# Performance work log

Hardware: AMD Instinct MI355X
Metric: run time of the kernel (lower is better)

Reference implementation:

```python
import jax, jax.numpy as jnp
import numpy as np
from jax import lax

REPR, ACT, HID = 256, 2, 512
BN_EPS = 1e-5


def setup_inputs() -> dict:
    key = jax.random.key(0)
    ks = jax.random.split(key, 12)
    B, H, W, Tm1 = 512, 64, 64, 16
    d_in = REPR + ACT
    s = lambda k, shape, scale: jax.random.normal(k, shape, dtype=jnp.float32) * scale
    return {
        "init_state": jax.random.normal(ks[0], (B, 2, H, W), dtype=jnp.float32),
        "actions": jax.random.normal(ks[1], (B, Tm1, ACT), dtype=jnp.float32),
        "conv_w": s(ks[2], (16, 2, 3, 3), (1.0 / np.sqrt(2 * 9))),
        "bn_gamma": jnp.ones((16,), jnp.float32),
        "bn_beta": jnp.zeros((16,), jnp.float32),
        "enc_fc_w": s(ks[3], (REPR, 16), (1.0 / np.sqrt(16))),
        "enc_fc_b": s(ks[4], (REPR,), 0.01),
        "gru_w_ih": s(ks[5], (3 * HID, d_in), (1.0 / np.sqrt(HID))),
        "gru_w_hh": s(ks[6], (3 * HID, HID), (1.0 / np.sqrt(HID))),
        "gru_b_ih": s(ks[7], (3 * HID,), (1.0 / np.sqrt(HID))),
        "gru_b_hh": s(ks[8], (3 * HID,), (1.0 / np.sqrt(HID))),
        "pred_fc_w": s(ks[9], (REPR, HID), (1.0 / np.sqrt(HID))),
        "pred_fc_b": s(ks[10], (REPR,), 0.01),
    }


def _encoder(x, conv_w, bn_gamma, bn_beta, enc_fc_w, enc_fc_b):
    # Conv2d(2->16, 3x3, stride 1, pad 1, no bias), NCHW
    y = lax.conv_general_dilated(x, conv_w, (1, 1), "SAME",
                                 dimension_numbers=("NCHW", "OIHW", "NCHW"))
    # BatchNorm2d in training mode: batch statistics over (N, H, W)
    mean = jnp.mean(y, axis=(0, 2, 3), keepdims=True)
    var = jnp.var(y, axis=(0, 2, 3), keepdims=True)
    y = (y - mean) * lax.rsqrt(var + BN_EPS)
    y = y * bn_gamma[None, :, None, None] + bn_beta[None, :, None, None]
    y = jax.nn.relu(y)
    # MaxPool2d(2, 2)
    y = lax.reduce_window(y, -jnp.inf, lax.max, (1, 1, 2, 2), (1, 1, 2, 2), "VALID")
    # AdaptiveAvgPool2d((1,1)) + flatten
    y = jnp.mean(y, axis=(2, 3))  # (B, 16)
    return y @ enc_fc_w.T + enc_fc_b  # (B, repr_dim)


def reference(init_state, actions, conv_w, bn_gamma, bn_beta, enc_fc_w, enc_fc_b,
              gru_w_ih, gru_w_hh, gru_b_ih, gru_b_hh, pred_fc_w, pred_fc_b):
    B = init_state.shape[0]
    s0 = _encoder(init_state, conv_w, bn_gamma, bn_beta, enc_fc_w, enc_fc_b)  # (B, R)

    def step(carry, u_t):
        s_prev, h = carry
        x = jnp.concatenate([s_prev, u_t], axis=-1)          # (B, R+A)
        gx = x @ gru_w_ih.T + gru_b_ih                        # (B, 3H)
        gh = h @ gru_w_hh.T + gru_b_hh                        # (B, 3H)
        gx_r, gx_z, gx_n = jnp.split(gx, 3, axis=-1)
        gh_r, gh_z, gh_n = jnp.split(gh, 3, axis=-1)
        r = jax.nn.sigmoid(gx_r + gh_r)
        z = jax.nn.sigmoid(gx_z + gh_z)
        n = jnp.tanh(gx_n + r * gh_n)
        h_new = (1.0 - z) * n + z * h
        s_pred = jax.nn.relu(h_new @ pred_fc_w.T + pred_fc_b)  # (B, R)
        return (s_pred, h_new), s_pred

    h0 = jnp.zeros((B, HID), dtype=s0.dtype)
    u_seq = jnp.transpose(actions, (1, 0, 2))  # (T-1, B, A)
    _, preds = lax.scan(step, (s0, h0), u_seq)  # preds: (T-1, B, R)
    pred_encs = jnp.concatenate([s0[None], preds], axis=0)  # (T, B, R)
    return jnp.transpose(pred_encs, (1, 0, 2))  # (B, T, R)
```

## Files before the change

### kernel.cpp

```cpp
#include <hip/hip_runtime.h>
#include <hip/hip_bf16.h>
#include <math.h>

#define TM1 16
#define TT 17

typedef __attribute__((ext_vector_type(8))) __bf16 bf16x8;
typedef __attribute__((ext_vector_type(4))) float f32x4;

#define OFF_BSTATS 0
#define OFF_SPB    16384
#define OFF_PWB    81920
#define OFF_WIHB   147456
#define OFF_WHHB   344064
#define OFF_HB     737280

__global__ __launch_bounds__(256) void enc_stats_prep(
    const float* __restrict__ x, const float* __restrict__ cw,
    float* __restrict__ bstats,
    const float* __restrict__ wih, const float* __restrict__ whh,
    const float* __restrict__ pw,
    __hip_bfloat16* __restrict__ wihb, __hip_bfloat16* __restrict__ whhb,
    __hip_bfloat16* __restrict__ pwb) {
  {
    const int n1 = 1536 * 256, n2 = 1536 * 512, n3 = 256 * 512;
    int i = blockIdx.x * 256 + threadIdx.x;
    int st = gridDim.x * 256;
    for (int j = i; j < n1 + n2 + n3; j += st) {
      if (j < n1) {
        int r = j >> 8, c = j & 255;
        wihb[j] = __float2bfloat16(wih[r * 258 + c]);
      } else if (j < n1 + n2) {
        int k = j - n1;
        whhb[k] = __float2bfloat16(whh[k]);
      } else {
        int k = j - n1 - n2;
        pwb[k] = __float2bfloat16(pw[k]);
      }
    }
  }

  __shared__ float imgp[2 * 66 * 66];
  __shared__ float reds[4][16], redq[4][16];
  const int b = blockIdx.x, tid = threadIdx.x;
  const int wv = tid >> 6;
  for (int i = tid; i < 2 * 66 * 66; i += 256) imgp[i] = 0.0f;
  __syncthreads();
  const float* xb = x + b * 8192;
  for (int i = tid; i < 8192; i += 256) {
    int ci = i >> 12, rem = i & 4095, y = rem >> 6, xx = rem & 63;
    imgp[ci * 4356 + (y + 1) * 66 + (xx + 1)] = xb[i];
  }
  __syncthreads();

  for (int c4 = 0; c4 < 4; ++c4) {
    float w0[18], w1[18], w2[18], w3[18];
#pragma unroll
    for (int k = 0; k < 18; ++k) {
      w0[k] = cw[(c4 * 4 + 0) * 18 + k];
      w1[k] = cw[(c4 * 4 + 1) * 18 + k];
      w2[k] = cw[(c4 * 4 + 2) * 18 + k];
      w3[k] = cw[(c4 * 4 + 3) * 18 + k];
    }
    float s0 = 0, s1 = 0, s2 = 0, s3 = 0, q0 = 0, q1 = 0, q2 = 0, q3 = 0;
    for (int p = tid; p < 4096; p += 256) {
      int y = p >> 6, xx = p & 63;
      float v[18];
#pragma unroll
      for (int ci = 0; ci < 2; ++ci)
#pragma unroll
        for (int dy = 0; dy < 3; ++dy)
#pragma unroll
          for (int dx = 0; dx < 3; ++dx)
            v[ci * 9 + dy * 3 + dx] = imgp[ci * 4356 + (y + dy) * 66 + (xx + dx)];
      float a0 = 0, a1 = 0, a2 = 0, a3 = 0;
#pragma unroll
      for (int k = 0; k < 18; ++k) {
        a0 = fmaf(w0[k], v[k], a0);
        a1 = fmaf(w1[k], v[k], a1);
        a2 = fmaf(w2[k], v[k], a2);
        a3 = fmaf(w3[k], v[k], a3);
      }
      s0 += a0; q0 = fmaf(a0, a0, q0);
      s1 += a1; q1 = fmaf(a1, a1, q1);
      s2 += a2; q2 = fmaf(a2, a2, q2);
      s3 += a3; q3 = fmaf(a3, a3, q3);
    }
#pragma unroll
    for (int off = 32; off >= 1; off >>= 1) {
      s0 += __shfl_down(s0, off); q0 += __shfl_down(q0, off);
      s1 += __shfl_down(s1, off); q1 += __shfl_down(q1, off);
      s2 += __shfl_down(s2, off); q2 += __shfl_down(q2, off);
      s3 += __shfl_down(s3, off); q3 += __shfl_down(q3, off);
    }
    if ((tid & 63) == 0) {
      reds[wv][c4 * 4 + 0] = s0; redq[wv][c4 * 4 + 0] = q0;
      reds[wv][c4 * 4 + 1] = s1; redq[wv][c4 * 4 + 1] = q1;
      reds[wv][c4 * 4 + 2] = s2; redq[wv][c4 * 4 + 2] = q2;
      reds[wv][c4 * 4 + 3] = s3; redq[wv][c4 * 4 + 3] = q3;
    }
  }
  __syncthreads();
  if (tid < 16)
    bstats[b * 32 + tid] = reds[0][tid] + reds[1][tid] + reds[2][tid] + reds[3][tid];
  else if (tid < 32) {
    int c = tid - 16;
    bstats[b * 32 + tid] = redq[0][c] + redq[1][c] + redq[2][c] + redq[3][c];
  }
}

__global__ __launch_bounds__(256) void enc_finish(const float* __restrict__ x,
                                                  const float* __restrict__ cw,
                                                  const float* __restrict__ bstats,
                                                  const float* __restrict__ gamma,
                                                  const float* __restrict__ beta,
                                                  const float* __restrict__ fcw,
                                                  const float* __restrict__ fcb,
                                                  __hip_bfloat16* __restrict__ spb,
                                                  float* __restrict__ out) {
  __shared__ float imgp[2 * 66 * 66];
  __shared__ float red[4][16];
  __shared__ float plds[16];
  __shared__ float statsL[32];
  __shared__ float racc[8][32];
  const int b = blockIdx.x, tid = threadIdx.x;

  {
    const int c = tid & 31, part = tid >> 5;
    float s = 0;
    for (int bb = part; bb < 512; bb += 8) s += bstats[bb * 32 + c];
    racc[part][c] = s;
  }
  for (int i = tid; i < 2 * 66 * 66; i += 256) imgp[i] = 0.0f;
  __syncthreads();
  if (tid < 32) {
    float v = 0;
#pragma unroll
    for (int p = 0; p < 8; ++p) v += racc[p][tid];
    statsL[tid] = v;
  }
  const float* xb = x + b * 8192;
  for (int i = tid; i < 8192; i += 256) {
    int ci = i >> 12, rem = i & 4095, y = rem >> 6, xx = rem & 63;
    imgp[ci * 4356 + (y + 1) * 66 + (xx + 1)] = xb[i];
  }
  __syncthreads();

  const float invN = 1.0f / (512.0f * 4096.0f);
  const int wv = tid >> 6;

  for (int c4 = 0; c4 < 4; ++c4) {
    float w0[18], w1[18], w2[18], w3[18];
#pragma unroll
    for (int k = 0; k < 18; ++k) {
      w0[k] = cw[(c4 * 4 + 0) * 18 + k];
      w1[k] = cw[(c4 * 4 + 1) * 18 + k];
      w2[k] = cw[(c4 * 4 + 2) * 18 + k];
      w3[k] = cw[(c4 * 4 + 3) * 18 + k];
    }
    float sc0, sc1, sc2, sc3, sh0, sh1, sh2, sh3;
    {
      int c = c4 * 4 + 0; float m = statsL[c] * invN; float var = statsL[16 + c] * invN - m * m;
      float isd = rsqrtf(var + 1e-5f); sc0 = gamma[c] * isd; sh0 = beta[c] - m * sc0;
      c = c4 * 4 + 1; m = statsL[c] * invN; var = statsL[16 + c] * invN - m * m;
      isd = rsqrtf(var + 1e-5f); sc1 = gamma[c] * isd; sh1 = beta[c] - m * sc1;
      c = c4 * 4 + 2; m = statsL[c] * invN; var = statsL[16 + c] * invN - m * m;
      isd = rsqrtf(var + 1e-5f); sc2 = gamma[c] * isd; sh2 = beta[c] - m * sc2;
      c = c4 * 4 + 3; m = statsL[c] * invN; var = statsL[16 + c] * invN - m * m;
      isd = rsqrtf(var + 1e-5f); sc3 = gamma[c] * isd; sh3 = beta[c] - m * sc3;
    }
    float p0 = 0, p1 = 0, p2 = 0, p3 = 0;
    for (int q = tid; q < 1024; q += 256) {
      int py = q >> 5, px = q & 31;
      float m0 = 0, m1 = 0, m2 = 0, m3 = 0;
#pragma unroll
      for (int sy = 0; sy < 2; ++sy)
#pragma unroll
        for (int sx = 0; sx < 2; ++sx) {
          int y = 2 * py + sy, xx = 2 * px + sx;
          float v[18];
#pragma unroll
          for (int ci = 0; ci < 2; ++ci)
#pragma unroll
            for (int dy = 0; dy < 3; ++dy)
#pragma unroll
              for (int dx = 0; dx < 3; ++dx)
                v[ci * 9 + dy * 3 + dx] = imgp[ci * 4356 + (y + dy) * 66 + (xx + dx)];
          float a0 = 0, a1 = 0, a2 = 0, a3 = 0;
#pragma unroll
          for (int k = 0; k < 18; ++k) {
            a0 = fmaf(w0[k], v[k], a0);
            a1 = fmaf(w1[k], v[k], a1);
            a2 = fmaf(w2[k], v[k], a2);
            a3 = fmaf(w3[k], v[k], a3);
          }
          m0 = fmaxf(m0, fmaxf(fmaf(a0, sc0, sh0), 0.0f));
          m1 = fmaxf(m1, fmaxf(fmaf(a1, sc1, sh1), 0.0f));
          m2 = fmaxf(m2, fmaxf(fmaf(a2, sc2, sh2), 0.0f));
          m3 = fmaxf(m3, fmaxf(fmaf(a3, sc3, sh3), 0.0f));
        }
      p0 += m0; p1 += m1; p2 += m2; p3 += m3;
    }
#pragma unroll
    for (int off = 32; off >= 1; off >>= 1) {
      p0 += __shfl_down(p0, off);
      p1 += __shfl_down(p1, off);
      p2 += __shfl_down(p2, off);
      p3 += __shfl_down(p3, off);
    }
    if ((tid & 63) == 0) {
      red[wv][c4 * 4 + 0] = p0;
      red[wv][c4 * 4 + 1] = p1;
      red[wv][c4 * 4 + 2] = p2;
      red[wv][c4 * 4 + 3] = p3;
    }
  }
  __syncthreads();
  if (tid < 16)
    plds[tid] = (red[0][tid] + red[1][tid] + red[2][tid] + red[3][tid]) * (1.0f / 1024.0f);
  __syncthreads();

  float acc = fcb[tid];
#pragma unroll
  for (int c = 0; c < 16; ++c) acc = fmaf(plds[c], fcw[tid * 16 + c], acc);
  spb[b * 256 + tid] = __float2bfloat16(acc);
  out[(b * TT + 0) * 256 + tid] = acc;
}

__global__ __launch_bounds__(384) void gru_v2(
    const __hip_bfloat16* __restrict__ spb,
    const __hip_bfloat16* __restrict__ hb_in,
    __hip_bfloat16* __restrict__ hb_out,
    const __hip_bfloat16* __restrict__ wihb,
    const __hip_bfloat16* __restrict__ whhb,
    const float* __restrict__ wih,
    const float* __restrict__ actions,
    const float* __restrict__ bih, const float* __restrict__ bhh,
    int t) {
  __shared__ __hip_bfloat16 sF[8 * 64 * 8];
  __shared__ __hip_bfloat16 hF[16 * 64 * 8];
  __shared__ float accL[4][2][256];
  const int tid = threadIdx.x;
  const int w = tid / 64, lane = tid & 63;
  const int l15 = lane & 15, hi = lane >> 4;
  const int cg = blockIdx.x, band = blockIdx.y;
  const int row0 = band * 16;
  const int ct = w & 1, g = w >> 1;

  for (int i = tid; i < 512; i += 384) {
    int kk = i >> 6, ln = i & 63;
    *(bf16x8*)(sF + i * 8) =
        *(const bf16x8*)(spb + (row0 + (ln & 15)) * 256 + kk * 32 + (ln >> 4) * 8);
  }
  if (t > 0) {
    for (int i = tid; i < 1024; i += 384) {
      int kk = i >> 6, ln = i & 63;
      *(bf16x8*)(hF + i * 8) =
          *(const bf16x8*)(hb_in + (row0 + (ln & 15)) * 512 + kk * 32 + (ln >> 4) * 8);
    }
  }
  __syncthreads();

  const int cj = cg * 32 + ct * 16;
  f32x4 accS = {0.f, 0.f, 0.f, 0.f}, accH = accS;
  {
    const __hip_bfloat16* B = wihb + (g * 512 + cj + l15) * 256 + hi * 8;
#pragma unroll
    for (int kk = 0; kk < 8; ++kk) {
      bf16x8 a = *(const bf16x8*)(sF + (kk * 64 + lane) * 8);
      accS = __builtin_amdgcn_mfma_f32_16x16x32_bf16(a, *(const bf16x8*)(B + kk * 32),
                                                     accS, 0, 0, 0);
    }
  }
  if (t > 0) {
    const __hip_bfloat16* B = whhb + (g * 512 + cj + l15) * 512 + hi * 8;
#pragma unroll
    for (int kk = 0; kk < 16; ++kk) {
      bf16x8 a = *(const bf16x8*)(hF + (kk * 64 + lane) * 8);
      accH = __builtin_amdgcn_mfma_f32_16x16x32_bf16(a, *(const bf16x8*)(B + kk * 32),
                                                     accH, 0, 0, 0);
    }
  }
  if (g < 2) {
#pragma unroll
    for (int i = 0; i < 4; ++i)
      accL[g][ct][(hi * 4 + i) * 16 + l15] = accS[i] + accH[i];
  } else {
#pragma unroll
    for (int i = 0; i < 4; ++i) {
      accL[2][ct][(hi * 4 + i) * 16 + l15] = accS[i];
      accL[3][ct][(hi * 4 + i) * 16 + l15] = accH[i];
    }
  }
  __syncthreads();

  if (w < 2) {
    f32x4 vR = *(const f32x4*)&accL[0][w][lane * 4];
    f32x4 vZ = *(const f32x4*)&accL[1][w][lane * 4];
    f32x4 vXN = *(const f32x4*)&accL[2][w][lane * 4];
    f32x4 vHN = *(const f32x4*)&accL[3][w][lane * 4];
    const int r = lane >> 2;
    const int row = row0 + r;
    const float u0 = actions[row * 32 + t * 2 + 0];
    const float u1 = actions[row * 32 + t * 2 + 1];
#pragma unroll
    for (int j = 0; j < 4; ++j) {
      const int c = (lane & 3) * 4 + j;
      const int col = cg * 32 + w * 16 + c;
      const float br = bih[col] + bhh[col];
      const float bz = bih[512 + col] + bhh[512 + col];
      const float bxn = bih[1024 + col];
      const float bhn = bhh[1024 + col];
      const float wur = wih[col * 258 + 256], wvr = wih[col * 258 + 257];
      const float wuz = wih[(512 + col) * 258 + 256], wvz = wih[(512 + col) * 258 + 257];
      const float wun = wih[(1024 + col) * 258 + 256], wvn = wih[(1024 + col) * 258 + 257];
      const float gr = vR[j] + br + u0 * wur + u1 * wvr;
      const float gz = vZ[j] + bz + u0 * wuz + u1 * wvz;
      const float gxn = vXN[j] + bxn + u0 * wun + u1 * wvn;
      const float ghn = vHN[j] + bhn;
      const float rg = 1.0f / (1.0f + __expf(-gr));
      const float zg = 1.0f / (1.0f + __expf(-gz));
      float xn = gxn + rg * ghn;
      xn = fminf(fmaxf(xn, -15.0f), 15.0f);
      const float e = __expf(2.0f * xn);
      const float ng = (e - 1.0f) / (e + 1.0f);
      const float hp = (t > 0) ? (float)hb_in[row * 512 + col] : 0.0f;
      const float hnv = (1.0f - zg) * ng + zg * hp;
      hb_out[row * 512 + col] = __float2bfloat16(hnv);
    }
  }
}

__global__ __launch_bounds__(256) void pred_v2(
    const __hip_bfloat16* __restrict__ hb,
    const __hip_bfloat16* __restrict__ pwb,
    const float* __restrict__ pb,
    float* __restrict__ out,
    __hip_bfloat16* __restrict__ spb,
    int slot) {
  __shared__ float accL[4][256];
  const int tid = threadIdx.x;
  const int w = tid >> 6, lane = tid & 63;
  const int l15 = lane & 15, hi = lane >> 4;
  const int pcg = blockIdx.x, band = blockIdx.y;
  const int row0 = band * 16, pc0 = pcg * 16;
  f32x4 acc = {0.f, 0.f, 0.f, 0.f};
  const __hip_bfloat16* A = hb + (row0 + l15) * 512 + w * 128 + hi * 8;
  const __hip_bfloat16* B = pwb + (pc0 + l15) * 512 + w * 128 + hi * 8;
#pragma unroll
  for (int kk = 0; kk < 4; ++kk)
    acc = __builtin_amdgcn_mfma_f32_16x16x32_bf16(*(const bf16x8*)(A + kk * 32),
                                                  *(const bf16x8*)(B + kk * 32),
                                                  acc, 0, 0, 0);
#pragma unroll
  for (int i = 0; i < 4; ++i) accL[w][(hi * 4 + i) * 16 + l15] = acc[i];
  __syncthreads();
  if (w == 0) {
    f32x4 p0 = *(const f32x4*)&accL[0][lane * 4];
    f32x4 p1 = *(const f32x4*)&accL[1][lane * 4];
    f32x4 p2 = *(const f32x4*)&accL[2][lane * 4];
    f32x4 p3 = *(const f32x4*)&accL[3][lane * 4];
    const int r = lane >> 2;
    const int row = row0 + r;
    float4 ov;
    float* po = &ov.x;
#pragma unroll
    for (int j = 0; j < 4; ++j) {
      const int c = (lane & 3) * 4 + j;
      const int col = pc0 + c;
      float v = p0[j] + p1[j] + p2[j] + p3[j] + pb[col];
      v = fmaxf(v, 0.0f);
      po[j] = v;
      spb[row * 256 + col] = __float2bfloat16(v);
    }
    *(float4*)(out + ((size_t)row * TT + slot) * 256 + pc0 + (lane & 3) * 4) = ov;
  }
}

extern "C" void kernel_launch(void* const* d_in, const int* in_sizes, int n_in,
                              void* d_out, int out_size, void* d_ws, size_t ws_size,
                              hipStream_t stream) {
  const float* x       = (const float*)d_in[0];
  const float* actions = (const float*)d_in[1];
  const float* cw      = (const float*)d_in[2];
  const float* gamma   = (const float*)d_in[3];
  const float* beta    = (const float*)d_in[4];
  const float* fcw     = (const float*)d_in[5];
  const float* fcb     = (const float*)d_in[6];
  const float* wih     = (const float*)d_in[7];
  const float* whh     = (const float*)d_in[8];
  const float* bih     = (const float*)d_in[9];
  const float* bhh     = (const float*)d_in[10];
  const float* pw      = (const float*)d_in[11];
  const float* pb      = (const float*)d_in[12];
  float* out = (float*)d_out;
  float* ws  = (float*)d_ws;

  float* bstats = ws + OFF_BSTATS;
  __hip_bfloat16* spb  = (__hip_bfloat16*)(ws + OFF_SPB);
  __hip_bfloat16* pwb  = (__hip_bfloat16*)(ws + OFF_PWB);
  __hip_bfloat16* wihb = (__hip_bfloat16*)(ws + OFF_WIHB);
  __hip_bfloat16* whhb = (__hip_bfloat16*)(ws + OFF_WHHB);
  __hip_bfloat16* hb0  = (__hip_bfloat16*)(ws + OFF_HB);
  __hip_bfloat16* hb1  = hb0 + 512 * 512;

  enc_stats_prep<<<dim3(512), dim3(256), 0, stream>>>(x, cw, bstats, wih, whh, pw,
                                                      wihb, whhb, pwb);
  enc_finish<<<dim3(512), dim3(256), 0, stream>>>(x, cw, bstats, gamma, beta, fcw, fcb,
                                                  spb, out);
  for (int t = 0; t < TM1; ++t) {
    __hip_bfloat16* hbi = (t & 1) ? hb1 : hb0;
    __hip_bfloat16* hbo = (t & 1) ? hb0 : hb1;
    gru_v2<<<dim3(16, 32), dim3(384), 0, stream>>>(spb, hbi, hbo, wihb, whhb,
                                                   wih, actions, bih, bhh, t);
    pred_v2<<<dim3(16, 32), dim3(256), 0, stream>>>(hbo, pwb, pb, out, spb, t + 1);
  }
}
```

Before: 356.1 us.

## Register-tile conv in encoder kernels to reuse LDS loads across output pixels

Both encoder kernels now give each thread a strip of output pixels: 8 consecutive columns in one row for the stats pass, and a 2x4 pooled patch for the finish pass. Input rows are loaded from LDS once and reused across neighboring outputs and four channels, which cuts LDS reads per FMA. Channel partial sums are kept in registers and reduced once at the end. This raises register pressure and can produce LDS bank conflicts from strided row accesses.

New measurement: 373.5 us. 4.9% more time.

```diff
diff --git a/kernel.cpp b/kernel.cpp
--- a/kernel.cpp
+++ b/kernel.cpp
@@ -53,52 +53,71 @@
   }
   __syncthreads();
 
-  for (int c4 = 0; c4 < 4; ++c4) {
-    float w0[18], w1[18], w2[18], w3[18];
-#pragma unroll
-    for (int k = 0; k < 18; ++k) {
-      w0[k] = cw[(c4 * 4 + 0) * 18 + k];
-      w1[k] = cw[(c4 * 4 + 1) * 18 + k];
-      w2[k] = cw[(c4 * 4 + 2) * 18 + k];
-      w3[k] = cw[(c4 * 4 + 3) * 18 + k];
-    }
-    float s0 = 0, s1 = 0, s2 = 0, s3 = 0, q0 = 0, q1 = 0, q2 = 0, q3 = 0;
-    for (int p = tid; p < 4096; p += 256) {
-      int y = p >> 6, xx = p & 63;
-      float v[18];
-#pragma unroll
-      for (int ci = 0; ci < 2; ++ci)
+  const int r = tid >> 2;
+  const int cs = (tid & 3) << 4;
+
+  float s[16], q[16];
+#pragma unroll
+  for (int c = 0; c < 16; ++c) { s[c] = 0.0f; q[c] = 0.0f; }
+
+#pragma unroll
+  for (int half = 0; half < 2; ++half) {
+    const int c0 = cs + half * 8;
+#pragma unroll
+    for (int c4 = 0; c4 < 4; ++c4) {
+      float a[4][8];
+#pragma unroll
+      for (int ch = 0; ch < 4; ++ch)
+#pragma unroll
+        for (int j = 0; j < 8; ++j) a[ch][j] = 0.0f;
+#pragma unroll
+      for (int ci = 0; ci < 2; ++ci) {
+        float wk[4][9];
+#pragma unroll
+        for (int ch = 0; ch < 4; ++ch)
+#pragma unroll
+          for (int k = 0; k < 9; ++k)
+            wk[ch][k] = cw[(c4 * 4 + ch) * 18 + ci * 9 + k];
+        float rv[3][10];
 #pragma unroll
         for (int dy = 0; dy < 3; ++dy)
 #pragma unroll
-          for (int dx = 0; dx < 3; ++dx)
-            v[ci * 9 + dy * 3 + dx] = imgp[ci * 4356 + (y + dy) * 66 + (xx + dx)];
-      float a0 = 0, a1 = 0, a2 = 0, a3 = 0;
-#pragma unroll
-      for (int k = 0; k < 18; ++k) {
-        a0 = fmaf(w0[k], v[k], a0);
-        a1 = fmaf(w1[k], v[k], a1);
-        a2 = fmaf(w2[k], v[k], a2);
-        a3 = fmaf(w3[k], v[k], a3);
+          for (int j = 0; j < 10; ++j)
+            rv[dy][j] = imgp[ci * 4356 + (r + dy) * 66 + c0 + j];
+#pragma unroll
+        for (int j = 0; j < 8; ++j)
+#pragma unroll
+          for (int ch = 0; ch < 4; ++ch) {
+            float acc = a[ch][j];
+#pragma unroll
+            for (int dy = 0; dy < 3; ++dy) {
+              acc = fmaf(wk[ch][dy * 3 + 0], rv[dy][j + 0], acc);
+              acc = fmaf(wk[ch][dy * 3 + 1], rv[dy][j + 1], acc);
+              acc = fmaf(wk[ch][dy * 3 + 2], rv[dy][j + 2], acc);
+            }
+            a[ch][j] = acc;
+          }
       }
-      s0 += a0; q0 = fmaf(a0, a0, q0);
-      s1 += a1; q1 = fmaf(a1, a1, q1);
-      s2 += a2; q2 = fmaf(a2, a2, q2);
-      s3 += a3; q3 = fmaf(a3, a3, q3);
-    }
+#pragma unroll
+      for (int ch = 0; ch < 4; ++ch)
+#pragma unroll
+        for (int j = 0; j < 8; ++j) {
+          const float v = a[ch][j];
+          s[c4 * 4 + ch] += v;
+          q[c4 * 4 + ch] = fmaf(v, v, q[c4 * 4 + ch]);
+        }
+    }
+  }
+
+#pragma unroll
+  for (int c = 0; c < 16; ++c) {
+    float sv = s[c], qv = q[c];
 #pragma unroll
     for (int off = 32; off >= 1; off >>= 1) {
-      s0 += __shfl_down(s0, off); q0 += __shfl_down(q0, off);
-      s1 += __shfl_down(s1, off); q1 += __shfl_down(q1, off);
-      s2 += __shfl_down(s2, off); q2 += __shfl_down(q2, off);
-      s3 += __shfl_down(s3, off); q3 += __shfl_down(q3, off);
-    }
-    if ((tid & 63) == 0) {
-      reds[wv][c4 * 4 + 0] = s0; redq[wv][c4 * 4 + 0] = q0;
-      reds[wv][c4 * 4 + 1] = s1; redq[wv][c4 * 4 + 1] = q1;
-      reds[wv][c4 * 4 + 2] = s2; redq[wv][c4 * 4 + 2] = q2;
-      reds[wv][c4 * 4 + 3] = s3; redq[wv][c4 * 4 + 3] = q3;
-    }
+      sv += __shfl_down(sv, off);
+      qv += __shfl_down(qv, off);
+    }
+    if ((tid & 63) == 0) { reds[wv][c] = sv; redq[wv][c] = qv; }
   }
   __syncthreads();
   if (tid < 16)
@@ -124,6 +143,7 @@
   __shared__ float statsL[32];
   __shared__ float racc[8][32];
   const int b = blockIdx.x, tid = threadIdx.x;
+  const int wv = tid >> 6;
 
   {
     const int c = tid & 31, part = tid >> 5;
@@ -147,73 +167,83 @@
   __syncthreads();
 
   const float invN = 1.0f / (512.0f * 4096.0f);
-  const int wv = tid >> 6;
-
+  const int py = tid >> 3;
+  const int ocs = (tid & 7) << 2;
+
+  float psum[16];
+#pragma unroll
+  for (int c = 0; c < 16; ++c) psum[c] = 0.0f;
+
+#pragma unroll
   for (int c4 = 0; c4 < 4; ++c4) {
-    float w0[18], w1[18], w2[18], w3[18];
-#pragma unroll
-    for (int k = 0; k < 18; ++k) {
-      w0[k] = cw[(c4 * 4 + 0) * 18 + k];
-      w1[k] = cw[(c4 * 4 + 1) * 18 + k];
-      w2[k] = cw[(c4 * 4 + 2) * 18 + k];
-      w3[k] = cw[(c4 * 4 + 3) * 18 + k];
-    }
-    float sc0, sc1, sc2, sc3, sh0, sh1, sh2, sh3;
-    {
-      int c = c4 * 4 + 0; float m = statsL[c] * invN; float var = statsL[16 + c] * invN - m * m;
-      float isd = rsqrtf(var + 1e-5f); sc0 = gamma[c] * isd; sh0 = beta[c] - m * sc0;
-      c = c4 * 4 + 1; m = statsL[c] * invN; var = statsL[16 + c] * invN - m * m;
-      isd = rsqrtf(var + 1e-5f); sc1 = gamma[c] * isd; sh1 = beta[c] - m * sc1;
-      c = c4 * 4 + 2; m = statsL[c] * invN; var = statsL[16 + c] * invN - m * m;
-      isd = rsqrtf(var + 1e-5f); sc2 = gamma[c] * isd; sh2 = beta[c] - m * sc2;
-      c = c4 * 4 + 3; m = statsL[c] * invN; var = statsL[16 + c] * invN - m * m;
-      isd = rsqrtf(var + 1e-5f); sc3 = gamma[c] * isd; sh3 = beta[c] - m * sc3;
-    }
-    float p0 = 0, p1 = 0, p2 = 0, p3 = 0;
-    for (int q = tid; q < 1024; q += 256) {
-      int py = q >> 5, px = q & 31;
-      float m0 = 0, m1 = 0, m2 = 0, m3 = 0;
-#pragma unroll
-      for (int sy = 0; sy < 2; ++sy)
-#pragma unroll
-        for (int sx = 0; sx < 2; ++sx) {
-          int y = 2 * py + sy, xx = 2 * px + sx;
-          float v[18];
-#pragma unroll
-          for (int ci = 0; ci < 2; ++ci)
-#pragma unroll
-            for (int dy = 0; dy < 3; ++dy)
-#pragma unroll
-              for (int dx = 0; dx < 3; ++dx)
-                v[ci * 9 + dy * 3 + dx] = imgp[ci * 4356 + (y + dy) * 66 + (xx + dx)];
-          float a0 = 0, a1 = 0, a2 = 0, a3 = 0;
-#pragma unroll
-          for (int k = 0; k < 18; ++k) {
-            a0 = fmaf(w0[k], v[k], a0);
-            a1 = fmaf(w1[k], v[k], a1);
-            a2 = fmaf(w2[k], v[k], a2);
-            a3 = fmaf(w3[k], v[k], a3);
-          }
-          m0 = fmaxf(m0, fmaxf(fmaf(a0, sc0, sh0), 0.0f));
-          m1 = fmaxf(m1, fmaxf(fmaf(a1, sc1, sh1), 0.0f));
-          m2 = fmaxf(m2, fmaxf(fmaf(a2, sc2, sh2), 0.0f));
-          m3 = fmaxf(m3, fmaxf(fmaf(a3, sc3, sh3), 0.0f));
+    float sc[4], sh[4];
+#pragma unroll
+    for (int ch = 0; ch < 4; ++ch) {
+      const int c = c4 * 4 + ch;
+      const float m = statsL[c] * invN;
+      const float var = statsL[16 + c] * invN - m * m;
+      const float isd = rsqrtf(var + 1e-5f);
+      sc[ch] = gamma[c] * isd;
+      sh[ch] = beta[c] - m * sc[ch];
+    }
+#pragma unroll
+    for (int op = 0; op < 2; ++op) {
+      const int oc = ocs + op * 2;
+      const int ic = oc * 2;
+      float a[4][8];
+#pragma unroll
+      for (int ch = 0; ch < 4; ++ch)
+#pragma unroll
+        for (int j = 0; j < 8; ++j) a[ch][j] = 0.0f;
+#pragma unroll
+      for (int ci = 0; ci < 2; ++ci) {
+        float wk[4][9];
+#pragma unroll
+        for (int ch = 0; ch < 4; ++ch)
+#pragma unroll
+          for (int k = 0; k < 9; ++k)
+            wk[ch][k] = cw[(c4 * 4 + ch) * 18 + ci * 9 + k];
+        float rv[4][6];
+#pragma unroll
+        for (int dy = 0; dy < 4; ++dy)
+#pragma unroll
+          for (int j = 0; j < 6; ++j)
+            rv[dy][j] = imgp[ci * 4356 + (2 * py + dy) * 66 + ic + j];
+#pragma unroll
+        for (int ry = 0; ry < 2; ++ry)
+#pragma unroll
+          for (int rx = 0; rx < 4; ++rx)
+#pragma unroll
+            for (int ch = 0; ch < 4; ++ch) {
+              float acc = a[ch][ry * 4 + rx];
+#pragma unroll
+              for (int dy = 0; dy < 3; ++dy) {
+                acc = fmaf(wk[ch][dy * 3 + 0], rv[ry + dy][rx + 0], acc);
+                acc = fmaf(wk[ch][dy * 3 + 1], rv[ry + dy][rx + 1], acc);
+                acc = fmaf(wk[ch][dy * 3 + 2], rv[ry + dy][rx + 2], acc);
+              }
+              a[ch][ry * 4 + rx] = acc;
+            }
+      }
+#pragma unroll
+      for (int ch = 0; ch < 4; ++ch)
+#pragma unroll
+        for (int j = 0; j < 2; ++j) {
+          const float v00 = fmaxf(fmaf(a[ch][2 * j + 0], sc[ch], sh[ch]), 0.0f);
+          const float v01 = fmaxf(fmaf(a[ch][2 * j + 1], sc[ch], sh[ch]), 0.0f);
+          const float v10 = fmaxf(fmaf(a[ch][4 + 2 * j + 0], sc[ch], sh[ch]), 0.0f);
+          const float v11 = fmaxf(fmaf(a[ch][4 + 2 * j + 1], sc[ch], sh[ch]), 0.0f);
+          psum[c4 * 4 + ch] += fmaxf(fmaxf(v00, v01), fmaxf(v10, v11));
         }
-      p0 += m0; p1 += m1; p2 += m2; p3 += m3;
-    }
-#pragma unroll
-    for (int off = 32; off >= 1; off >>= 1) {
-      p0 += __shfl_down(p0, off);
-      p1 += __shfl_down(p1, off);
-      p2 += __shfl_down(p2, off);
-      p3 += __shfl_down(p3, off);
-    }
-    if ((tid & 63) == 0) {
-      red[wv][c4 * 4 + 0] = p0;
-      red[wv][c4 * 4 + 1] = p1;
-      red[wv][c4 * 4 + 2] = p2;
-      red[wv][c4 * 4 + 3] = p3;
-    }
+    }
+  }
+
+#pragma unroll
+  for (int c = 0; c < 16; ++c) {
+    float v = psum[c];
+#pragma unroll
+    for (int off = 32; off >= 1; off >>= 1) v += __shfl_down(v, off);
+    if ((tid & 63) == 0) red[wv][c] = v;
   }
   __syncthreads();
   if (tid < 16)
```
